# Kernel tuning notes

Measured on AMD Instinct MI355X. Metric: run time of the kernel, lower is better.

## Reference

```python
import jax, jax.numpy as jnp
import numpy as np

NTOKEN, NINP, NHID, NLAYERS = 33278, 400, 1150, 3


def _lstm_scan(x_seq, h0, c0, Wih, Whh, bih, bhh):
    # x_seq: [T,B,in], h0/c0: [B,H]; PyTorch gate order i,f,g,o
    def step(carry, x):
        h, c = carry
        gates = x @ Wih.T + bih + h @ Whh.T + bhh  # [B,4H]
        i, f, g, o = jnp.split(gates, 4, axis=-1)
        c = jax.nn.sigmoid(f) * c + jax.nn.sigmoid(i) * jnp.tanh(g)
        h = jax.nn.sigmoid(o) * jnp.tanh(c)
        return (h, c), h
    (hT, cT), hs = jax.lax.scan(step, (h0, c0), x_seq)
    return hs, hT, cT


def _causal_attention(hs):
    # hs: [T,B,H]; dot-product attention of h_t over h_{0..t} (causal)
    T = hs.shape[0]
    scores = jnp.einsum('tbh,sbh->bts', hs, hs)  # [B,T,T]
    mask = jnp.tril(jnp.ones((T, T), dtype=bool))
    scores = jnp.where(mask[None, :, :], scores, -1e30)
    attn = jax.nn.softmax(scores, axis=-1)
    return jnp.einsum('bts,sbh->tbh', attn, hs)


def setup_inputs() -> dict:
    key = jax.random.key(0)
    ks = jax.random.split(key, 24)
    T, B = 100, 64
    inp = {
        'input': jax.random.randint(ks[0], (T, B), 0, NTOKEN),
        'input2': jax.random.randint(ks[1], (T, B), 0, NTOKEN),
        'h0': jnp.zeros((1, B, NHID)), 'c0': jnp.zeros((1, B, NHID)),
        'h1': jnp.zeros((1, B, NHID)), 'c1': jnp.zeros((1, B, NHID)),
        'h2': jnp.zeros((1, B, NHID)), 'c2': jnp.zeros((1, B, NHID)),
    }
    inp['emb_W'] = jax.random.uniform(ks[2], (NTOKEN, NINP), minval=-0.1, maxval=0.1)
    in_sizes = [2 * NINP, NHID, NHID]
    for l in range(NLAYERS):
        s = 1.0 / np.sqrt(NHID)
        inp[f'W_ih{l}'] = jax.random.uniform(ks[3 + 4 * l], (4 * NHID, in_sizes[l]), minval=-s, maxval=s)
        inp[f'W_hh{l}'] = jax.random.uniform(ks[4 + 4 * l], (4 * NHID, NHID), minval=-s, maxval=s)
        inp[f'b_ih{l}'] = jax.random.uniform(ks[5 + 4 * l], (4 * NHID,), minval=-s, maxval=s)
        inp[f'b_hh{l}'] = jax.random.uniform(ks[6 + 4 * l], (4 * NHID,), minval=-s, maxval=s)
    inp['dec_W'] = jax.random.uniform(ks[20], (NTOKEN, NHID), minval=-0.1, maxval=0.1)
    inp['dec_b'] = jnp.zeros((NTOKEN,))
    return inp


def reference(input, input2, h0, c0, h1, c1, h2, c2, emb_W,
              W_ih0, W_hh0, b_ih0, b_hh0,
              W_ih1, W_hh1, b_ih1, b_hh1,
              W_ih2, W_hh2, b_ih2, b_hh2,
              dec_W, dec_b):
    # eval mode: all dropouts are identity
    emb = jnp.concatenate([emb_W[input], emb_W[input2]], axis=-1)  # [T,B,2*ninp]
    x = emb
    hcs = [(h0[0], c0[0]), (h1[0], c1[0]), (h2[0], c2[0])]
    params = [(W_ih0, W_hh0, b_ih0, b_hh0), (W_ih1, W_hh1, b_ih1, b_hh1), (W_ih2, W_hh2, b_ih2, b_hh2)]
    for l in range(NLAYERS):
        hs, hT, cT = _lstm_scan(x, hcs[l][0], hcs[l][1], *params[l])
        if l == NLAYERS - 1:
            out = _causal_attention(hs)  # attention only on last layer
        else:
            x = hs
    T, B, H = out.shape
    decoded = out.reshape(T * B, H) @ dec_W.T + dec_b  # [T*B, ntoken]
    return decoded
```

## Files before the change

### kernel.cpp

```cpp
#include <hip/hip_runtime.h>
#include <stdint.h>

typedef unsigned short ushort_t;
typedef __bf16 bf16x8 __attribute__((ext_vector_type(8)));
typedef float f32x4 __attribute__((ext_vector_type(4)));

__device__ __forceinline__ float b2f(ushort_t u) {
  union { unsigned u; float f; } v; v.u = ((unsigned)u) << 16; return v.f;
}
__device__ __forceinline__ ushort_t f2b(float f) {
  union { float f; unsigned u; } v; v.f = f;
  unsigned r = (v.u + 0x7FFFu + ((v.u >> 16) & 1u)) >> 16;
  return (ushort_t)r;
}

__device__ __forceinline__ float sigm(float x)     { return 1.f / (1.f + __expf(-x)); }
__device__ __forceinline__ float tanhfast(float x) { return 1.f - 2.f / (1.f + __expf(2.f * x)); }

__device__ __forceinline__ void store_short_wt(ushort_t* p, ushort_t v) {
  asm volatile("global_store_short %0, %1, off sc0 sc1"
               :: "v"(p), "v"((unsigned)v) : "memory");
}
__device__ __forceinline__ void store_uint_wt(unsigned* p, unsigned v) {
  asm volatile("global_store_dword %0, %1, off sc0 sc1"
               :: "v"(p), "v"(v) : "memory");
}

__device__ __forceinline__ void gload_lds16(const void* g, void* lds) {
  auto l3 = reinterpret_cast<__attribute__((address_space(3))) unsigned*>(
      reinterpret_cast<uintptr_t>(lds));
  __builtin_amdgcn_global_load_lds(reinterpret_cast<const unsigned*>(g), l3, 16, 0, 0);
}

template <bool F32OUT>
__global__ __launch_bounds__(512) void gemm_bt(
    const ushort_t* __restrict__ A, const ushort_t* __restrict__ B,
    void* __restrict__ Cv,
    const float* __restrict__ bias0, const float* __restrict__ bias1,
    int lda, int ldb, long ldc, int Kpad, int N)
{
  __shared__ alignas(16) ushort_t As[256 * 32];
  __shared__ alignas(16) ushort_t Bs[256 * 32];
  const int tid = threadIdx.x;
  const int w = tid >> 6, l = tid & 63;
  const int wr = w >> 2, wc = w & 3;

  unsigned nwg = gridDim.x * gridDim.y;
  unsigned wg = blockIdx.y * gridDim.x + blockIdx.x;
  {
    unsigned q = nwg >> 3, r = nwg & 7u;
    unsigned xcd = wg & 7u, idx = wg >> 3;
    wg = (xcd < r ? xcd * (q + 1) : r * (q + 1) + (xcd - r) * q) + idx;
  }
  const long m0 = (long)(wg % gridDim.x) * 256;
  const long n0 = (long)(wg / gridDim.x) * 256;

  const int lrow = l & 15, hi = l >> 4, lk = hi * 8;

  f32x4 acc[8][4] = {};

  const int c0 = tid, c1 = tid + 512;
  const int r0 = c0 >> 2, g0 = (c0 & 3) * 8;
  const int r1 = c1 >> 2, g1 = (c1 & 3) * 8;

  for (int k0 = 0; k0 < Kpad; k0 += 32) {
    gload_lds16(A + (m0 + r0) * lda + k0 + g0, As + c0 * 8);
    gload_lds16(A + (m0 + r1) * lda + k0 + g1, As + c1 * 8);
    gload_lds16(B + (n0 + r0) * ldb + k0 + g0, Bs + c0 * 8);
    gload_lds16(B + (n0 + r1) * ldb + k0 + g1, Bs + c1 * 8);
    __syncthreads();

    bf16x8 af[8], bfr[4];
#pragma unroll
    for (int mi = 0; mi < 8; mi++)
      af[mi] = *(const bf16x8*)(As + (wr * 128 + mi * 16 + lrow) * 32 + lk);
#pragma unroll
    for (int ni = 0; ni < 4; ni++)
      bfr[ni] = *(const bf16x8*)(Bs + (wc * 64 + ni * 16 + lrow) * 32 + lk);
#pragma unroll
    for (int mi = 0; mi < 8; mi++)
#pragma unroll
      for (int ni = 0; ni < 4; ni++)
        acc[mi][ni] = __builtin_amdgcn_mfma_f32_16x16x32_bf16(af[mi], bfr[ni], acc[mi][ni], 0, 0, 0);
    __syncthreads();
  }

  const int rbase = hi * 4;
#pragma unroll
  for (int ni = 0; ni < 4; ni++) {
    int gcol = (int)n0 + wc * 64 + ni * 16 + lrow;
    if (gcol < N) {
      float badd = 0.f;
      if (bias0) badd += bias0[gcol];
      if (bias1) badd += bias1[gcol];
#pragma unroll
      for (int mi = 0; mi < 8; mi++) {
#pragma unroll
        for (int r = 0; r < 4; r++) {
          long grow = m0 + wr * 128 + mi * 16 + rbase + r;
          float v = acc[mi][ni][r] + badd;
          if (F32OUT) ((float*)Cv)[grow * ldc + gcol] = v;
          else        ((ushort_t*)Cv)[grow * ldc + gcol] = f2b(v);
        }
      }
    }
  }
}

__global__ __launch_bounds__(256) void lstm_layer(
    ushort_t* __restrict__ hs,
    const ushort_t* __restrict__ G,
    const ushort_t* __restrict__ Whh,
    const float* __restrict__ c_in,
    unsigned* __restrict__ flags)
{
  extern __shared__ ushort_t Bsh[];
  const int tid = threadIdx.x;
  const int w = tid >> 6, l = tid & 63;
  const int us = blockIdx.x;
  const int lrow = l & 15, hi = l >> 4, lk = hi * 8;
  const int u = us * 16 + lrow;
  const int usafe = (u < 1150) ? u : 0;
  const int row0 = w * 16 + hi * 4;
  const int x7 = lrow & 7;
  const int start = us >> 1;

  for (int ci = tid; ci < 9216; ci += 256) {
    int gate = ci / 2304;
    int rem  = ci - gate * 2304;
    int row  = rem / 144;
    int c    = rem - row * 144;
    bf16x8 v = *(const bf16x8*)(Whh + ((long)(gate * 1150 + us * 16 + row)) * 1152 + c * 8);
    *(bf16x8*)(Bsh + (((gate * 16 + row) * 144) + (c ^ (row & 7))) * 8) = v;
  }
  const ushort_t* Bg0 = Bsh + ((0 * 16 + lrow) * 144) * 8;
  const ushort_t* Bg1 = Bsh + ((1 * 16 + lrow) * 144) * 8;
  const ushort_t* Bg2 = Bsh + ((2 * 16 + lrow) * 144) * 8;
  const ushort_t* Bg3 = Bsh + ((3 * 16 + lrow) * 144) * 8;

  f32x4 cc = {};
  if (u < 1150) {
#pragma unroll
    for (int r = 0; r < 4; ++r) cc[r] = c_in[(row0 + r) * 1150 + u];
  }
  __syncthreads();

  const int s1 = l, s2 = 64 + (l & 7);

  for (int t = 0; t < 100; ++t) {
    ushort_t gvv[16];
    {
      const ushort_t* gp = G + ((long)t * 64 + row0) * 4608 + usafe;
#pragma unroll
      for (int r = 0; r < 4; ++r)
#pragma unroll
        for (int g = 0; g < 4; ++g)
          gvv[r * 4 + g] = gp[(long)r * 4608 + g * 1150];
    }

    if (t > 0) {
      if (w == 0) {
        const unsigned tt = (unsigned)t;
        unsigned f1 = (s1 == us) ? tt :
            __hip_atomic_load(flags + (s1 << 5), __ATOMIC_RELAXED, __HIP_MEMORY_SCOPE_AGENT);
        unsigned f2 = (s2 == us) ? tt :
            __hip_atomic_load(flags + (s2 << 5), __ATOMIC_RELAXED, __HIP_MEMORY_SCOPE_AGENT);
        unsigned long long p1 = __ballot(f1 >= tt);
        unsigned long long p2 = __ballot(f2 >= tt);
        while ((p1 & p2) != ~0ull) {
          __builtin_amdgcn_s_sleep(8);
          if (!((p1 >> l) & 1))
            f1 = __hip_atomic_load(flags + (s1 << 5), __ATOMIC_RELAXED, __HIP_MEMORY_SCOPE_AGENT);
          if (!((p2 >> l) & 1))
            f2 = __hip_atomic_load(flags + (s2 << 5), __ATOMIC_RELAXED, __HIP_MEMORY_SCOPE_AGENT);
          p1 = __ballot(f1 >= tt);
          p2 = __ballot(f2 >= tt);
        }
      }
      __syncthreads();
      asm volatile("" ::: "memory");
    }

    const ushort_t* hp = hs + (long)t * 73728 + (long)(w * 16 + lrow) * 1152 + lk;
    f32x4 a0 = {}, a1 = {}, a2 = {}, a3 = {};

    bf16x8 A0[9], A1[9];
    auto ldg = [&](bf16x8* buf, int g) {
#pragma unroll
      for (int i = 0; i < 9; ++i) {
        int kc = start + g * 9 + i; if (kc >= 36) kc -= 36;
        buf[i] = *(const bf16x8*)(hp + kc * 32);
      }
    };
    auto cons = [&](const bf16x8* buf, int g) {
#pragma unroll
      for (int i = 0; i < 9; ++i) {
        int kc = start + g * 9 + i; if (kc >= 36) kc -= 36;
        int pc8 = ((kc * 4 + hi) ^ x7) * 8;
        a0 = __builtin_amdgcn_mfma_f32_16x16x32_bf16(buf[i], *(const bf16x8*)(Bg0 + pc8), a0, 0, 0, 0);
        a1 = __builtin_amdgcn_mfma_f32_16x16x32_bf16(buf[i], *(const bf16x8*)(Bg1 + pc8), a1, 0, 0, 0);
        a2 = __builtin_amdgcn_mfma_f32_16x16x32_bf16(buf[i], *(const bf16x8*)(Bg2 + pc8), a2, 0, 0, 0);
        a3 = __builtin_amdgcn_mfma_f32_16x16x32_bf16(buf[i], *(const bf16x8*)(Bg3 + pc8), a3, 0, 0, 0);
      }
    };
    ldg(A0, 0); ldg(A1, 1);
    cons(A0, 0); ldg(A0, 2);
    cons(A1, 1); ldg(A1, 3);
    cons(A0, 2);
    cons(A1, 3);

    if (u < 1150) {
#pragma unroll
      for (int r = 0; r < 4; ++r) {
        float iv = a0[r] + b2f(gvv[r * 4 + 0]);
        float fv = a1[r] + b2f(gvv[r * 4 + 1]);
        float gg = a2[r] + b2f(gvv[r * 4 + 2]);
        float ov = a3[r] + b2f(gvv[r * 4 + 3]);
        float cn = sigm(fv) * cc[r] + sigm(iv) * tanhfast(gg);
        cc[r] = cn;
        float hv = sigm(ov) * tanhfast(cn);
        store_short_wt(hs + (long)(t + 1) * 73728 + (long)(row0 + r) * 1152 + u, f2b(hv));
      }
    }

    if (t != 99) {
      asm volatile("s_waitcnt vmcnt(0)" ::: "memory");
      __syncthreads();
      if (tid == 0) store_uint_wt(flags + (us << 5), (unsigned)(t + 1));
    }
  }
}

__global__ __launch_bounds__(256) void attn_kernel(
    const ushort_t* __restrict__ hs2,
    ushort_t* __restrict__ outp)
{
  __shared__ float qf[1152];
  __shared__ float sc[104];
  __shared__ float sinv;
  const int rowi = blockIdx.x;
  const int t = rowi >> 6, b = rowi & 63;
  const int tid = threadIdx.x;
  const int w = tid >> 6, l = tid & 63;

  const ushort_t* q = hs2 + (long)rowi * 1152;
  for (int c = tid; c < 1150; c += 256) qf[c] = b2f(q[c]);
  __syncthreads();

  for (int s = w; s <= t; s += 4) {
    const ushort_t* k = hs2 + (long)(s * 64 + b) * 1152;
    float p = 0.f;
    for (int h = l; h < 1150; h += 64) p += qf[h] * b2f(k[h]);
    for (int off = 32; off; off >>= 1) p += __shfl_down(p, off);
    if (l == 0) sc[s] = p;
  }
  __syncthreads();

  if (w == 0) {
    float m = -1e30f;
    for (int s = l; s <= t; s += 64) m = fmaxf(m, sc[s]);
    for (int off = 32; off; off >>= 1) m = fmaxf(m, __shfl_down(m, off));
    m = __shfl(m, 0);
    float sum = 0.f;
    for (int s = l; s <= t; s += 64) { float e = __expf(sc[s] - m); sc[s] = e; sum += e; }
    for (int off = 32; off; off >>= 1) sum += __shfl_down(sum, off);
    if (l == 0) sinv = 1.f / sum;
  }
  __syncthreads();

  const float si = sinv;
  for (int h = tid; h < 1150; h += 256) {
    float a = 0.f;
    for (int s = 0; s <= t; s++) a += sc[s] * b2f(hs2[(long)(s * 64 + b) * 1152 + h]);
    outp[(long)rowi * 1152 + h] = f2b(a * si);
  }
  if (tid < 2) outp[(long)rowi * 1152 + 1150 + tid] = 0;
}

__global__ void embed_kernel(const int* __restrict__ in1, const int* __restrict__ in2,
                             const float* __restrict__ emb, ushort_t* __restrict__ x0)
{
  int rowi = blockIdx.x;
  int l = threadIdx.x;
  long r1 = (long)in1[rowi] * 400, r2 = (long)in2[rowi] * 400;
  ushort_t* d = x0 + (long)rowi * 800;
  for (int c = l; c < 800; c += 64)
    d[c] = f2b(c < 400 ? emb[r1 + c] : emb[r2 + c - 400]);
}

__global__ void pad_convert(const float* __restrict__ in, ushort_t* __restrict__ out,
                            int R, int Cin, int total, int Cp)
{
  int idx = blockIdx.x * 256 + threadIdx.x;
  if (idx >= total) return;
  int r = idx / Cp, c = idx - r * Cp;
  float v = (r < R && c < Cin) ? in[(long)r * Cin + c] : 0.f;
  out[idx] = f2b(v);
}

__global__ void init_state(const float* __restrict__ h_in,
                           ushort_t* __restrict__ hs, unsigned* __restrict__ flags)
{
  int idx = blockIdx.x * 256 + threadIdx.x;
  if (idx < 72 * 32) flags[idx] = 0u;
  if (idx < 64 * 1152) {
    int b = idx / 1152, c = idx - b * 1152;
    hs[idx] = (c < 1150) ? f2b(h_in[b * 1150 + c]) : (ushort_t)0;
  }
  if (idx < 100 * 128) {
    int t = idx >> 7, r = idx & 127, b = r >> 1, k = r & 1;
    hs[(long)(t + 1) * 73728 + b * 1152 + 1150 + k] = 0;
  }
}

extern "C" void kernel_launch(void* const* d_in, const int* in_sizes, int n_in,
                              void* d_out, int out_size, void* d_ws, size_t ws_size,
                              hipStream_t stream) {
  (void)in_sizes; (void)n_in; (void)out_size; (void)ws_size;
  const int* input  = (const int*)d_in[0];
  const int* input2 = (const int*)d_in[1];
  const float* h_in[3] = {(const float*)d_in[2], (const float*)d_in[4], (const float*)d_in[6]};
  const float* c_in[3] = {(const float*)d_in[3], (const float*)d_in[5], (const float*)d_in[7]};
  const float* emb_W = (const float*)d_in[8];
  const float* W_ih[3] = {(const float*)d_in[9],  (const float*)d_in[13], (const float*)d_in[17]};
  const float* W_hh[3] = {(const float*)d_in[10], (const float*)d_in[14], (const float*)d_in[18]};
  const float* b_ih[3] = {(const float*)d_in[11], (const float*)d_in[15], (const float*)d_in[19]};
  const float* b_hh[3] = {(const float*)d_in[12], (const float*)d_in[16], (const float*)d_in[20]};
  const float* dec_W = (const float*)d_in[21];
  const float* dec_b = (const float*)d_in[22];
  float* out = (float*)d_out;

  hipFuncSetAttribute((const void*)lstm_layer,
                      hipFuncAttributeMaxDynamicSharedMemorySize, 147456);

  char* base = (char*)d_ws;
  size_t off = 0;
  auto walloc = [&](size_t bytes) { char* r = base + off; off += (bytes + 255) & ~(size_t)255; return r; };
  ushort_t* decWp = (ushort_t*)walloc(33280ull * 1152 * 2);
  ushort_t* attnB = (ushort_t*)walloc(6400ull * 1152 * 2);
  unsigned* flags = (unsigned*)walloc(72 * 128 + 256);

  char* ob = (char*)d_out;
  ushort_t* G   = (ushort_t*)(ob + 0);
  ushort_t* x0  = (ushort_t*)(ob + 58982400);
  ushort_t* Wp  = (ushort_t*)(ob + 69222400);
  ushort_t* Whp = (ushort_t*)(ob + 79839232);
  ushort_t* hsA = (ushort_t*)(ob + 90456064);
  ushort_t* hsB = (ushort_t*)(ob + 105349120);

  embed_kernel<<<6400, 64, 0, stream>>>(input, input2, emb_W, x0);

  ushort_t* hcur[3] = {hsA, hsB, hsA};
  const ushort_t* X = x0;
  int lda = 800, Kp = 800;
  for (int lyr = 0; lyr < 3; lyr++) {
    if (lyr == 0) {
      int tot = 4608 * 800;
      pad_convert<<<(tot + 255) / 256, 256, 0, stream>>>(W_ih[0], Wp, 4600, 800, tot, 800);
    } else {
      int tot = 4608 * 1152;
      pad_convert<<<(tot + 255) / 256, 256, 0, stream>>>(W_ih[lyr], Wp, 4600, 1150, tot, 1152);
    }
    {
      int tot = 4608 * 1152;
      pad_convert<<<(tot + 255) / 256, 256, 0, stream>>>(W_hh[lyr], Whp, 4600, 1150, tot, 1152);
    }
    gemm_bt<false><<<dim3(25, 18), 512, 0, stream>>>(X, Wp, (void*)G, b_ih[lyr], b_hh[lyr],
                                                     lda, Kp, 4608L, Kp, 4600);
    init_state<<<288, 256, 0, stream>>>(h_in[lyr], hcur[lyr], flags);
    lstm_layer<<<72, 256, 147456, stream>>>(hcur[lyr], G, Whp, c_in[lyr], flags);
    X = hcur[lyr] + 73728;
    lda = 1152; Kp = 1152;
  }

  attn_kernel<<<6400, 256, 0, stream>>>(hsA + 73728, attnB);

  {
    int tot = 33280 * 1152;
    pad_convert<<<(tot + 255) / 256, 256, 0, stream>>>(dec_W, decWp, 33278, 1150, tot, 1152);
  }

  gemm_bt<true><<<dim3(25, 130), 512, 0, stream>>>(attnB, decWp, (void*)out, dec_b, nullptr,
                                                   1152, 1152, 33278L, 1152, 33278);
}
```

Baseline: 3.681 ms.

## Double-buffer GEMM with BK=64, XOR-swizzled LDS, and async prefetch

Rewrites the 256x256 GEMM main loop to stage K-tiles of 64 into two dynamic-LDS buffers, prefetching tile t+2 while computing tile t, with partial vmcnt waits instead of a full sync per step. LDS rows are XOR-swizzled to cut bank conflicts on the bf16x8 fragment reads, and MFMA sections run at raised wave priority. Layer-0 input and weights are padded from K=800 to 832 so K divides by 64, which shifts scratch buffer offsets inside the output. The 128KB LDS footprint limits occupancy to one block per CU, and the padding adds a little extra arithmetic.

```diff
diff --git a/kernel.cpp b/kernel.cpp
--- a/kernel.cpp
+++ b/kernel.cpp
@@ -32,18 +32,25 @@
   __builtin_amdgcn_global_load_lds(reinterpret_cast<const unsigned*>(g), l3, 16, 0, 0);
 }
 
+__device__ __forceinline__ void rbar() {
+  asm volatile("" ::: "memory");
+  __builtin_amdgcn_s_barrier();
+  asm volatile("" ::: "memory");
+}
+
 template <bool F32OUT>
-__global__ __launch_bounds__(512) void gemm_bt(
+__global__ __launch_bounds__(512) void gemm256(
     const ushort_t* __restrict__ A, const ushort_t* __restrict__ B,
     void* __restrict__ Cv,
     const float* __restrict__ bias0, const float* __restrict__ bias1,
     int lda, int ldb, long ldc, int Kpad, int N)
 {
-  __shared__ alignas(16) ushort_t As[256 * 32];
-  __shared__ alignas(16) ushort_t Bs[256 * 32];
+  extern __shared__ ushort_t sh[];
   const int tid = threadIdx.x;
   const int w = tid >> 6, l = tid & 63;
   const int wr = w >> 2, wc = w & 3;
+  const int lrow = l & 15, hi = l >> 4;
+  const int xsw = (lrow & 7) << 3;
 
   unsigned nwg = gridDim.x * gridDim.y;
   unsigned wg = blockIdx.y * gridDim.x + blockIdx.x;
@@ -55,34 +62,65 @@
   const long m0 = (long)(wg % gridDim.x) * 256;
   const long n0 = (long)(wg / gridDim.x) * 256;
 
-  const int lrow = l & 15, hi = l >> 4, lk = hi * 8;
+  int crow[4], csrc[4];
+#pragma unroll
+  for (int j = 0; j < 4; ++j) {
+    int c = tid + j * 512;
+    crow[j] = c >> 3;
+    csrc[j] = ((c & 7) * 8) ^ ((crow[j] & 7) << 3);
+  }
+
+  auto STAGE = [&](int buf, int t) {
+    const long k0 = (long)t * 64;
+    ushort_t* dstA = sh + buf * 32768;
+    ushort_t* dstB = dstA + 16384;
+#pragma unroll
+    for (int j = 0; j < 4; ++j)
+      gload_lds16(A + (m0 + crow[j]) * lda + k0 + csrc[j], dstA + (tid + j * 512) * 8);
+#pragma unroll
+    for (int j = 0; j < 4; ++j)
+      gload_lds16(B + (n0 + crow[j]) * ldb + k0 + csrc[j], dstB + (tid + j * 512) * 8);
+  };
 
   f32x4 acc[8][4] = {};
-
-  const int c0 = tid, c1 = tid + 512;
-  const int r0 = c0 >> 2, g0 = (c0 & 3) * 8;
-  const int r1 = c1 >> 2, g1 = (c1 & 3) * 8;
-
-  for (int k0 = 0; k0 < Kpad; k0 += 32) {
-    gload_lds16(A + (m0 + r0) * lda + k0 + g0, As + c0 * 8);
-    gload_lds16(A + (m0 + r1) * lda + k0 + g1, As + c1 * 8);
-    gload_lds16(B + (n0 + r0) * ldb + k0 + g0, Bs + c0 * 8);
-    gload_lds16(B + (n0 + r1) * ldb + k0 + g1, Bs + c1 * 8);
-    __syncthreads();
-
-    bf16x8 af[8], bfr[4];
-#pragma unroll
-    for (int mi = 0; mi < 8; mi++)
-      af[mi] = *(const bf16x8*)(As + (wr * 128 + mi * 16 + lrow) * 32 + lk);
-#pragma unroll
-    for (int ni = 0; ni < 4; ni++)
-      bfr[ni] = *(const bf16x8*)(Bs + (wc * 64 + ni * 16 + lrow) * 32 + lk);
-#pragma unroll
-    for (int mi = 0; mi < 8; mi++)
-#pragma unroll
-      for (int ni = 0; ni < 4; ni++)
-        acc[mi][ni] = __builtin_amdgcn_mfma_f32_16x16x32_bf16(af[mi], bfr[ni], acc[mi][ni], 0, 0, 0);
-    __syncthreads();
+  const int nt = Kpad >> 6;
+
+  STAGE(0, 0);
+  STAGE(1, 1);
+  asm volatile("s_waitcnt vmcnt(8)" ::: "memory");
+  rbar();
+
+  for (int t = 0; t < nt; ++t) {
+    const ushort_t* As = sh + (t & 1) * 32768;
+    const ushort_t* Bs = As + 16384;
+#pragma unroll
+    for (int kk = 0; kk < 2; ++kk) {
+      bf16x8 af[8], bfr[4];
+      const int co = (kk * 32 + hi * 8) ^ xsw;
+#pragma unroll
+      for (int mi = 0; mi < 8; ++mi)
+        af[mi] = *(const bf16x8*)(As + (wr * 128 + mi * 16 + lrow) * 64 + co);
+#pragma unroll
+      for (int ni = 0; ni < 4; ++ni)
+        bfr[ni] = *(const bf16x8*)(Bs + (wc * 64 + ni * 16 + lrow) * 64 + co);
+      __builtin_amdgcn_s_setprio(1);
+#pragma unroll
+      for (int mi = 0; mi < 8; ++mi)
+#pragma unroll
+        for (int ni = 0; ni < 4; ++ni)
+          acc[mi][ni] = __builtin_amdgcn_mfma_f32_16x16x32_bf16(af[mi], bfr[ni], acc[mi][ni], 0, 0, 0);
+      __builtin_amdgcn_s_setprio(0);
+    }
+    if (t + 2 < nt) {
+      rbar();
+      STAGE(t & 1, t + 2);
+      asm volatile("s_waitcnt vmcnt(8)" ::: "memory");
+      rbar();
+    } else if (t + 1 < nt) {
+      rbar();
+      asm volatile("s_waitcnt vmcnt(0)" ::: "memory");
+      rbar();
+    }
   }
 
   const int rbase = hi * 4;
@@ -283,9 +321,12 @@
   int rowi = blockIdx.x;
   int l = threadIdx.x;
   long r1 = (long)in1[rowi] * 400, r2 = (long)in2[rowi] * 400;
-  ushort_t* d = x0 + (long)rowi * 800;
-  for (int c = l; c < 800; c += 64)
-    d[c] = f2b(c < 400 ? emb[r1 + c] : emb[r2 + c - 400]);
+  ushort_t* d = x0 + (long)rowi * 832;
+  for (int c = l; c < 832; c += 64) {
+    ushort_t v = 0;
+    if (c < 800) v = f2b(c < 400 ? emb[r1 + c] : emb[r2 + c - 400]);
+    d[c] = v;
+  }
 }
 
 __global__ void pad_convert(const float* __restrict__ in, ushort_t* __restrict__ out,
@@ -332,6 +373,10 @@
 
   hipFuncSetAttribute((const void*)lstm_layer,
                       hipFuncAttributeMaxDynamicSharedMemorySize, 147456);
+  hipFuncSetAttribute(reinterpret_cast<const void*>(gemm256<false>),
+                      hipFuncAttributeMaxDynamicSharedMemorySize, 131072);
+  hipFuncSetAttribute(reinterpret_cast<const void*>(gemm256<true>),
+                      hipFuncAttributeMaxDynamicSharedMemorySize, 131072);
 
   char* base = (char*)d_ws;
   size_t off = 0;
@@ -343,20 +388,20 @@
   char* ob = (char*)d_out;
   ushort_t* G   = (ushort_t*)(ob + 0);
   ushort_t* x0  = (ushort_t*)(ob + 58982400);
-  ushort_t* Wp  = (ushort_t*)(ob + 69222400);
-  ushort_t* Whp = (ushort_t*)(ob + 79839232);
-  ushort_t* hsA = (ushort_t*)(ob + 90456064);
-  ushort_t* hsB = (ushort_t*)(ob + 105349120);
+  ushort_t* Wp  = (ushort_t*)(ob + 69632000);
+  ushort_t* Whp = (ushort_t*)(ob + 80248832);
+  ushort_t* hsA = (ushort_t*)(ob + 90865664);
+  ushort_t* hsB = (ushort_t*)(ob + 105758720);
 
   embed_kernel<<<6400, 64, 0, stream>>>(input, input2, emb_W, x0);
 
   ushort_t* hcur[3] = {hsA, hsB, hsA};
   const ushort_t* X = x0;
-  int lda = 800, Kp = 800;
+  int lda = 832, Kp = 832;
   for (int lyr = 0; lyr < 3; lyr++) {
     if (lyr == 0) {
-      int tot = 4608 * 800;
-      pad_convert<<<(tot + 255) / 256, 256, 0, stream>>>(W_ih[0], Wp, 4600, 800, tot, 800);
+      int tot = 4608 * 832;
+      pad_convert<<<(tot + 255) / 256, 256, 0, stream>>>(W_ih[0], Wp, 4600, 800, tot, 832);
     } else {
       int tot = 4608 * 1152;
       pad_convert<<<(tot + 255) / 256, 256, 0, stream>>>(W_ih[lyr], Wp, 4600, 1150, tot, 1152);
@@ -365,8 +410,8 @@
       int tot = 4608 * 1152;
       pad_convert<<<(tot + 255) / 256, 256, 0, stream>>>(W_hh[lyr], Whp, 4600, 1150, tot, 1152);
     }
-    gemm_bt<false><<<dim3(25, 18), 512, 0, stream>>>(X, Wp, (void*)G, b_ih[lyr], b_hh[lyr],
-                                                     lda, Kp, 4608L, Kp, 4600);
+    gemm256<false><<<dim3(25, 18), 512, 131072, stream>>>(X, Wp, (void*)G, b_ih[lyr], b_hh[lyr],
+                                                          lda, Kp, 4608L, Kp, 4600);
     init_state<<<288, 256, 0, stream>>>(h_in[lyr], hcur[lyr], flags);
     lstm_layer<<<72, 256, 147456, stream>>>(hcur[lyr], G, Whp, c_in[lyr], flags);
     X = hcur[lyr] + 73728;
@@ -380,6 +425,6 @@
     pad_convert<<<(tot + 255) / 256, 256, 0, stream>>>(dec_W, decWp, 33278, 1150, tot, 1152);
   }
 
-  gemm_bt<true><<<dim3(25, 130), 512, 0, stream>>>(attnB, decWp, (void*)out, dec_b, nullptr,
-                                                   1152, 1152, 33278L, 1152, 33278);
-}
+  gemm256<true><<<dim3(25, 130), 512, 131072, stream>>>(attnB, decWp, (void*)out, dec_b, nullptr,
+                                                        1152, 1152, 33278L, 1152, 33278);
+}
```

Measured after the change: 3.355 ms. 8.8% less time.
